# Optimization experiments

Hardware: AMD Instinct MI355X
Metric: run time of the kernel (lower is better)

Reference implementation:

```python
import jax, jax.numpy as jnp
import numpy as np

N, E, ND, D = 100000, 200000, 128, 32


def linear_bn(x, W, g, b, eps=1e-5):
    # Linear (no bias) followed by BatchNorm1d in training mode (batch stats)
    y = x @ W
    mu = jnp.mean(y, axis=0)
    var = jnp.var(y, axis=0)
    return g * (y - mu) * jax.lax.rsqrt(var + eps) + b


def setup_inputs() -> dict:
    key = jax.random.key(0)
    ks = jax.random.split(key, 16)
    s = 0.05
    return {
        "node": jax.random.normal(ks[0], (N, ND), jnp.float32),
        "edge_index": jax.random.randint(ks[1], (E, 2), 0, N, jnp.int64),
        "edge": jax.random.normal(ks[2], (E, D), jnp.float32),
        "hidden": jax.random.normal(ks[3], (1, E, D), jnp.float32),
        "W1": jax.random.normal(ks[4], (2 * ND, 256), jnp.float32) * s,
        "g1": jnp.ones((256,), jnp.float32), "b1": jnp.zeros((256,), jnp.float32),
        "W2": jax.random.normal(ks[5], (256, 256), jnp.float32) * s,
        "g2": jnp.ones((256,), jnp.float32), "b2": jnp.zeros((256,), jnp.float32),
        "W3": jax.random.normal(ks[6], (256, 128), jnp.float32) * s,
        "g3": jnp.ones((128,), jnp.float32), "b3": jnp.zeros((128,), jnp.float32),
        "W4": jax.random.normal(ks[7], (128, D * D), jnp.float32) * s,
        "g4": jnp.ones((D * D,), jnp.float32), "b4": jnp.zeros((D * D,), jnp.float32),
        "bias": jax.random.uniform(ks[8], (D,), jnp.float32, -1.0 / np.sqrt(D), 1.0 / np.sqrt(D)),
        "W_ih": jax.random.normal(ks[9], (3 * D, D), jnp.float32) * s,
        "W_hh": jax.random.normal(ks[10], (3 * D, D), jnp.float32) * s,
        "b_ih": jnp.zeros((3 * D,), jnp.float32),
        "b_hh": jnp.zeros((3 * D,), jnp.float32),
    }


def reference(node, edge_index, edge, hidden, W1, g1, b1, W2, g2, b2, W3, g3, b3,
              W4, g4, b4, bias, W_ih, W_hh, b_ih, b_hh):
    num_edge, edge_dim = edge.shape
    # gather endpoint node features and concat -> [E, 2*node_dim]
    x_ij = jnp.concatenate([node[edge_index[:, 0]], node[edge_index[:, 1]]], axis=1)
    h = jax.nn.relu(linear_bn(x_ij, W1, g1, b1))
    h = jax.nn.relu(linear_bn(h, W2, g2, b2))
    h = jax.nn.relu(linear_bn(h, W3, g3, b3))
    A = linear_bn(h, W4, g4, b4).reshape(num_edge, edge_dim, edge_dim)
    # per-edge small matmul: [E,1,D] @ [E,D,D] -> [E,D]
    message = jnp.einsum('ed,edf->ef', edge, A)
    message = jax.nn.relu(message + bias)
    # single-step GRU (seq_len=1, edges as batch)
    h0 = hidden[0]
    gi = message @ W_ih.T + b_ih
    gh = h0 @ W_hh.T + b_hh
    i_r, i_z, i_n = jnp.split(gi, 3, axis=1)
    h_r, h_z, h_n = jnp.split(gh, 3, axis=1)
    r = jax.nn.sigmoid(i_r + h_r)
    z = jax.nn.sigmoid(i_z + h_z)
    n = jnp.tanh(i_n + r * h_n)
    h_new = (1.0 - z) * n + z * h0
    return h_new, h_new[None]
```

## Files before the change

kernel.cpp:

```cpp
#include <hip/hip_runtime.h>
#include <hip/hip_fp16.h>

#define NE 200000
#define NT 6250
#define NT64 3125
#define GRAM_BLOCKS 512

__device__ float g_st[21248];
__device__ unsigned short g_c4h[1024];
__device__ int g_flag64;

#define SUM1 (&g_st[0])
#define SQ1  (&g_st[256])
#define SUM2 (&g_st[512])
#define SQ2  (&g_st[768])
#define SUM3 (&g_st[1024])
#define SQ3  (&g_st[1152])
#define GMAT (&g_st[1280])
#define CS3  (&g_st[17664])
#define A1   (&g_st[17792])
#define C1   (&g_st[18048])
#define A2   (&g_st[18304])
#define C2   (&g_st[18560])
#define A3   (&g_st[18816])
#define C3   (&g_st[18944])
#define A4   (&g_st[19072])
#define C4   (&g_st[20096])

typedef unsigned short u16;
typedef _Float16 f16x8 __attribute__((ext_vector_type(8)));
typedef float f32x4 __attribute__((ext_vector_type(4)));

__device__ __forceinline__ f32x4 mfma16(f16x8 a, f16x8 b, f32x4 c) {
  return __builtin_amdgcn_mfma_f32_16x16x32_f16(a, b, c, 0, 0, 0);
}
__device__ __forceinline__ u16 f2h(float x) {
  __half h = __float2half_rn(x);
  return *reinterpret_cast<u16*>(&h);
}
__device__ __forceinline__ float h2f(u16 s) {
  __half h = *reinterpret_cast<__half*>(&s);
  return __half2float(h);
}
__device__ __forceinline__ float relu_np(float t) { return (t < 0.f) ? 0.f : t; }
__device__ __forceinline__ unsigned packh2(float a, float b) {
  return (unsigned)f2h(a) | ((unsigned)f2h(b) << 16);
}

__global__ void GraphConv2_16518444221042_kernel(float* __restrict__ out,
                                                 float v, int n) {
  int i = blockIdx.x * 256 + threadIdx.x;
  if (i < n) out[i] = v;
}

__global__ void k_init(const int* __restrict__ e) {
  int i = blockIdx.x * 256 + threadIdx.x;
  if (i < 17792) g_st[i] = 0.f;
  if (i == 0) {
    int allz = 1;
    for (int k = 1; k < 128; k += 2) allz &= (e[k] == 0);
    g_flag64 = allz;
  }
}

__global__ void k_packA(const float* __restrict__ W1,
                        const float* __restrict__ W2,
                        const float* __restrict__ W3,
                        u16* __restrict__ dst) {
  int i = blockIdx.x * 256 + threadIdx.x;
  if (i >= 163840) return;
  float v;
  if (i < 65536) {
    int n = i >> 8, k = i & 255;
    v = W1[k * 256 + n];
  } else if (i < 131072) {
    int i2 = i - 65536, n = i2 >> 8, k = i2 & 255;
    v = W2[k * 256 + n];
  } else {
    int i2 = i - 131072, n = i2 >> 8, k = i2 & 255;
    v = W3[k * 128 + n];
  }
  dst[i] = f2h(v);
}

__global__ void k_packB(const float* __restrict__ W4,
                        const float* __restrict__ Wih,
                        const float* __restrict__ Whh,
                        u16* __restrict__ dst) {
  int i = blockIdx.x * 256 + threadIdx.x;
  if (i >= 137216) return;
  float v;
  if (i < 131072) {
    int n = i >> 7, k = i & 127;
    v = W4[(size_t)k * 1024 + n];
  } else if (i < 134144) {
    v = Wih[i - 131072];
  } else {
    v = Whh[i - 134144];
  }
  dst[i] = f2h(v);
}

__global__ void k_finalize(const float* __restrict__ g,
                           const float* __restrict__ b, int which, int C) {
  int j = threadIdx.x;
  if (j < C) {
    const float* sum = (which == 1) ? SUM1 : (which == 2) ? SUM2 : SUM3;
    const float* sq  = (which == 1) ? SQ1 : (which == 2) ? SQ2 : SQ3;
    float* aa = (which == 1) ? A1 : (which == 2) ? A2 : A3;
    float* cc = (which == 1) ? C1 : (which == 2) ? C2 : C3;
    const float invE = 1.f / (float)NE;
    float mu = sum[j] * invE;
    float var = fmaf(-mu, mu, sq[j] * invE);
    float s = rsqrtf(var + 1e-5f);
    float av = g[j] * s;
    aa[j] = av;
    cc[j] = fmaf(-av, mu, b[j]);
  }
}

__global__ __launch_bounds__(64) void k_finalize4(
    const float* __restrict__ W4, const float* __restrict__ g4,
    const float* __restrict__ b4) {
  __shared__ float wsh[128];
  const int lane = threadIdx.x;
  const float invE = 1.f / (float)NE;
  for (int j = blockIdx.x; j < 1024; j += gridDim.x) {
    float w0 = W4[lane * 1024 + j];
    float w1 = W4[(lane + 64) * 1024 + j];
    wsh[lane] = w0;
    wsh[lane + 64] = w1;
    __syncthreads();
    float s0 = 0.f, s1 = 0.f;
#pragma unroll 8
    for (int k = 0; k < 128; ++k) {
      float wk = wsh[k];
      s0 = fmaf(GMAT[lane * 128 + k], wk, s0);
      s1 = fmaf(GMAT[(lane + 64) * 128 + k], wk, s1);
    }
    float acc = w0 * s0 + w1 * s1;
    float mac = CS3[lane] * w0 + CS3[lane + 64] * w1;
#pragma unroll
    for (int off = 32; off > 0; off >>= 1) {
      acc += __shfl_down(acc, off);
      mac += __shfl_down(mac, off);
    }
    if (lane == 0) {
      float mu = mac * invE;
      float var = fmaf(-mu, mu, acc * invE);
      float s = rsqrtf(var + 1e-5f);
      float av = g4[j] * s;
      A4[j] = av;
      float cv = fmaf(-av, mu, b4[j]);
      C4[j] = cv;
      g_c4h[(j & 31) * 32 + (j >> 5)] = f2h(cv);
    }
    __syncthreads();
  }
}

template <int L>
__global__ __launch_bounds__(512) void k_gemmP(
    const float* __restrict__ node, const int* __restrict__ eidx,
    const u16* __restrict__ Yin, const u16* __restrict__ Wt,
    u16* __restrict__ Yout) {
  constexpr int CN = (L == 3) ? 128 : 256;
  constexpr int CTW = CN / 128;
  constexpr int LDH = 264;
  __shared__ __align__(16) u16 H[64 * LDH];
  __shared__ float csum_s[CN], csq_s[CN];
  __shared__ int idx_s[128];
  const int tid = threadIdx.x;
  float* SUMo = (L == 1) ? SUM1 : (L == 2) ? SUM2 : SUM3;
  float* SQo  = (L == 1) ? SQ1 : (L == 2) ? SQ2 : SQ3;
  const float* Ain = (L == 2) ? A1 : A2;
  const float* Cin = (L == 2) ? C1 : C2;

  const int l = tid & 63, w = tid >> 6;
  const int lr = l & 15, lg = l >> 4;

  f16x8 bfr[CTW][8];
#pragma unroll
  for (int c = 0; c < CTW; ++c)
#pragma unroll
    for (int kb = 0; kb < 8; ++kb)
      bfr[c][kb] = *(const f16x8*)&Wt[(size_t)((w * CTW + c) * 16 + lr) * 256 +
                                      kb * 32 + lg * 8];

  if (tid < CN) { csum_s[tid] = 0.f; csq_s[tid] = 0.f; }
  float sreg[CTW] = {}, qreg[CTW] = {};

  for (int t = blockIdx.x; t < NT64; t += gridDim.x) {
    const int r0 = t * 64;
    __syncthreads();
    if constexpr (L == 1) {
      if (tid < 128) {
        const int is64 = g_flag64;
        int m = tid & 63, sel = tid >> 6;
        int j = (r0 + m) * 2 + sel;
        int v = is64 ? eidx[j * 2] : eidx[j];
        v = v < 0 ? 0 : (v > 99999 ? 99999 : v);
        idx_s[sel * 64 + m] = v;
      }
      __syncthreads();
#pragma unroll
      for (int i = 0; i < 8; ++i) {
        int idx = tid + i * 512;
        int row = idx >> 6, col = (idx & 63) * 4;
        int sel = col >> 7, kc = col & 127;
        float4 v =
            *(const float4*)&node[(size_t)idx_s[sel * 64 + row] * 128 + kc];
        uint2 pk;
        pk.x = packh2(v.x, v.y);
        pk.y = packh2(v.z, v.w);
        *(uint2*)&H[row * LDH + col] = pk;
      }
    } else {
#pragma unroll
      for (int i = 0; i < 4; ++i) {
        int idx = tid + i * 512;
        int row = idx >> 5, col = (idx & 31) * 8;
        uint4 ld = *(const uint4*)&Yin[(size_t)(r0 + row) * 256 + col];
        const u16* sp = (const u16*)&ld;
        uint4 o;
        unsigned po[4];
#pragma unroll
        for (int p = 0; p < 4; ++p) {
          float v0 = relu_np(fmaf(Ain[col + 2 * p], h2f(sp[2 * p]),
                                  Cin[col + 2 * p]));
          float v1 = relu_np(fmaf(Ain[col + 2 * p + 1], h2f(sp[2 * p + 1]),
                                  Cin[col + 2 * p + 1]));
          po[p] = packh2(v0, v1);
        }
        o.x = po[0]; o.y = po[1]; o.z = po[2]; o.w = po[3];
        *(uint4*)&H[row * LDH + col] = o;
      }
    }
    __syncthreads();

    f32x4 acc[4][CTW] = {};
#pragma unroll
    for (int kb = 0; kb < 8; ++kb) {
      f16x8 a[4];
#pragma unroll
      for (int rt = 0; rt < 4; ++rt)
        a[rt] = *(const f16x8*)&H[(rt * 16 + lr) * LDH + kb * 32 + lg * 8];
#pragma unroll
      for (int c = 0; c < CTW; ++c)
#pragma unroll
        for (int rt = 0; rt < 4; ++rt)
          acc[rt][c] = mfma16(a[rt], bfr[c][kb], acc[rt][c]);
    }

#pragma unroll
    for (int c = 0; c < CTW; ++c) {
      const int col = (w * CTW + c) * 16 + lr;
#pragma unroll
      for (int rt = 0; rt < 4; ++rt)
#pragma unroll
        for (int r = 0; r < 4; ++r) {
          float v = acc[rt][c][r];
          sreg[c] += v;
          qreg[c] = fmaf(v, v, qreg[c]);
          int row = rt * 16 + lg * 4 + r;
          Yout[(size_t)(r0 + row) * CN + col] = f2h(v);
        }
    }
  }

  __syncthreads();
#pragma unroll
  for (int c = 0; c < CTW; ++c) {
    const int col = (w * CTW + c) * 16 + lr;
    atomicAdd(&csum_s[col], sreg[c]);
    atomicAdd(&csq_s[col], qreg[c]);
  }
  __syncthreads();
  if (tid < CN) {
    atomicAdd(&SUMo[tid], csum_s[tid]);
    atomicAdd(&SQo[tid], csq_s[tid]);
  }
}

__global__ __launch_bounds__(256, 2) void k_gram_m(const u16* __restrict__ y3g,
                                                   float* __restrict__ pg) {
  __shared__ u16 h3T[128 * 40];
  __shared__ float cred[128];
  const int tid = threadIdx.x;
  const int l = tid & 63, w = tid >> 6;
  const int lr = l & 15, lg = l >> 4;
  const int c4 = (tid & 31) * 4;
  const int rb = tid >> 5;
  f32x4 acc[2][8] = {};
  float csc[4] = {0.f, 0.f, 0.f, 0.f};

  for (int t = blockIdx.x; t < NT; t += gridDim.x) {
    const size_t r0 = (size_t)t * 32;
    __syncthreads();
#pragma unroll
    for (int i = 0; i < 4; ++i) {
      int row = rb + i * 8;
      ushort4 v = *(const ushort4*)&y3g[(r0 + row) * 128 + c4];
      float h[4];
      h[0] = relu_np(fmaf(A3[c4 + 0], h2f(v.x), C3[c4 + 0]));
      h[1] = relu_np(fmaf(A3[c4 + 1], h2f(v.y), C3[c4 + 1]));
      h[2] = relu_np(fmaf(A3[c4 + 2], h2f(v.z), C3[c4 + 2]));
      h[3] = relu_np(fmaf(A3[c4 + 3], h2f(v.w), C3[c4 + 3]));
#pragma unroll
      for (int j = 0; j < 4; ++j) {
        csc[j] += h[j];
        int col = c4 + j;
        int swz = ((col >> 2) & 3) << 3;
        h3T[col * 40 + (row ^ swz)] = f2h(h[j]);
      }
    }
    __syncthreads();
    f16x8 bfr[8];
#pragma unroll
    for (int tj = 0; tj < 8; ++tj) {
      int col = tj * 16 + lr;
      int swz = ((col >> 2) & 3) << 3;
      bfr[tj] = *(const f16x8*)&h3T[col * 40 + ((lg * 8) ^ swz)];
    }
#pragma unroll
    for (int ri = 0; ri < 2; ++ri) {
      f16x8 a = bfr[w * 2 + ri];
#pragma unroll
      for (int tj = 0; tj < 8; ++tj)
        acc[ri][tj] = mfma16(a, bfr[tj], acc[ri][tj]);
    }
  }
  float* my = pg + (size_t)blockIdx.x * 16384;
#pragma unroll
  for (int ri = 0; ri < 2; ++ri)
#pragma unroll
    for (int tj = 0; tj < 8; ++tj)
#pragma unroll
      for (int r = 0; r < 4; ++r) {
        int row = (w * 2 + ri) * 16 + lg * 4 + r, col = tj * 16 + lr;
        my[row * 128 + col] = acc[ri][tj][r];
      }
  if (tid < 128) cred[tid] = 0.f;
  __syncthreads();
#pragma unroll
  for (int j = 0; j < 4; ++j) atomicAdd(&cred[c4 + j], csc[j]);
  __syncthreads();
  if (tid < 128) atomicAdd(&CS3[tid], cred[tid]);
}

__global__ void k_gramred(const float* __restrict__ pg) {
  int g = blockIdx.x * 256 + threadIdx.x;
  float s = 0.f;
  for (int p = 0; p < GRAM_BLOCKS; ++p) s += pg[(size_t)p * 16384 + g];
  GMAT[g] = s;
}

__global__ __launch_bounds__(256, 4) void k_final64(
    const u16* __restrict__ y3g, const u16* __restrict__ w4t,
    const u16* __restrict__ wihh, const u16* __restrict__ whhh,
    const float* __restrict__ edge, const float* __restrict__ hidden,
    const float* __restrict__ bias, const float* __restrict__ bih,
    const float* __restrict__ bhh, float* __restrict__ out) {
  __shared__ __align__(16) u16 H3[64 * 136];
  __shared__ __align__(16) u16 SLAB[32 * 136];
  __shared__ __align__(16) u16 EDS[64 * 40];
  float* OUTBUF = (float*)H3;
  u16* MSGu = H3 + 4096;
  const int tid = threadIdx.x;
  const size_t r0 = (size_t)blockIdx.x * 64;

#pragma unroll
  for (int i = 0; i < 8; ++i) {
    int idx = tid + i * 256;
    int row = idx >> 5, col = (idx & 31) * 4;
    ushort4 v = *(const ushort4*)&y3g[(r0 + row) * 128 + col];
    float h0 = relu_np(fmaf(A3[col + 0], h2f(v.x), C3[col + 0]));
    float h1 = relu_np(fmaf(A3[col + 1], h2f(v.y), C3[col + 1]));
    float h2v = relu_np(fmaf(A3[col + 2], h2f(v.z), C3[col + 2]));
    float h3v = relu_np(fmaf(A3[col + 3], h2f(v.w), C3[col + 3]));
    uint2 pk;
    pk.x = packh2(h0, h1);
    pk.y = packh2(h2v, h3v);
    *(uint2*)&H3[row * 136 + col] = pk;
  }
#pragma unroll
  for (int i = 0; i < 2; ++i) {
    int idx = tid + i * 256;
    int row = idx >> 3, col = (idx & 7) * 4;
    float4 ev = *(const float4*)&edge[(r0 + row) * 32 + col];
    uint2 pe;
    pe.x = packh2(ev.x, ev.y);
    pe.y = packh2(ev.z, ev.w);
    *(uint2*)&EDS[row * 40 + col] = pe;
  }
  __syncthreads();

  const int l = tid & 63, w = tid >> 6;
  const int lr = l & 15, lg = l >> 4;
  f16x8 af[4];
#pragma unroll
  for (int kb = 0; kb < 4; ++kb)
    af[kb] = *(const f16x8*)&H3[(w * 16 + lr) * 136 + kb * 32 + lg * 8];

  float mp[4][2] = {};
  for (int cg = 0; cg < 32; ++cg) {
    __syncthreads();
    {
      int c = tid >> 3, ch = tid & 7;
#pragma unroll
      for (int q = 0; q < 2; ++q) {
        int kk = (ch + q * 8) * 8;
        *(uint4*)&SLAB[c * 136 + kk] =
            *(const uint4*)&w4t[(size_t)(cg * 32 + c) * 128 + kk];
      }
    }
    __syncthreads();
#pragma unroll
    for (int ci = 0; ci < 2; ++ci) {
      f16x8 b[4];
#pragma unroll
      for (int kb = 0; kb < 4; ++kb)
        b[kb] = *(const f16x8*)&SLAB[(ci * 16 + lr) * 136 + kb * 32 + lg * 8];
      const float a4v = A4[cg * 32 + ci * 16 + lr];
      f32x4 acc = {0.f, 0.f, 0.f, 0.f};
#pragma unroll
      for (int kb = 0; kb < 4; ++kb) acc = mfma16(af[kb], b[kb], acc);
#pragma unroll
      for (int r = 0; r < 4; ++r) {
        int e = w * 16 + lg * 4 + r;
        float ed = h2f(EDS[e * 40 + cg]);
        mp[r][ci] = fmaf(ed * a4v, acc[r], mp[r][ci]);
      }
    }
  }

  f32x4 m0[2];
  {
    f16x8 ae = *(const f16x8*)&EDS[(w * 16 + lr) * 40 + lg * 8];
#pragma unroll
    for (int ci = 0; ci < 2; ++ci) {
      f16x8 bc = *(const f16x8*)&g_c4h[(ci * 16 + lr) * 32 + lg * 8];
      f32x4 z = {0.f, 0.f, 0.f, 0.f};
      m0[ci] = mfma16(ae, bc, z);
    }
  }
#pragma unroll
  for (int ci = 0; ci < 2; ++ci)
#pragma unroll
    for (int r = 0; r < 4; ++r) {
      int e = w * 16 + lg * 4 + r;
      int f = ci * 16 + lr;
      float v = relu_np(mp[r][ci] + m0[ci][r] + bias[f]);
      MSGu[e * 40 + f] = f2h(v);
    }
  __syncthreads();

  f16x8 am = *(const f16x8*)&MSGu[(w * 16 + lr) * 40 + lg * 8];
  f16x8 ah;
  {
    int e = w * 16 + lr;
    float4 h0a = *(const float4*)&hidden[(r0 + e) * 32 + lg * 8];
    float4 h0b = *(const float4*)&hidden[(r0 + e) * 32 + lg * 8 + 4];
    union { unsigned u[4]; f16x8 h; } uu;
    uu.u[0] = packh2(h0a.x, h0a.y);
    uu.u[1] = packh2(h0a.z, h0a.w);
    uu.u[2] = packh2(h0b.x, h0b.y);
    uu.u[3] = packh2(h0b.z, h0b.w);
    ah = uu.h;
  }
  f32x4 gi[6], gh[6];
#pragma unroll
  for (int ct = 0; ct < 6; ++ct) {
    f16x8 bi = *(const f16x8*)&wihh[(ct * 16 + lr) * 32 + lg * 8];
    f16x8 bh = *(const f16x8*)&whhh[(ct * 16 + lr) * 32 + lg * 8];
    f32x4 z = {0.f, 0.f, 0.f, 0.f};
    gi[ct] = mfma16(am, bi, z);
    gh[ct] = mfma16(ah, bh, z);
  }
#pragma unroll
  for (int r = 0; r < 4; ++r) {
    int e = w * 16 + lg * 4 + r;
#pragma unroll
    for (int hf = 0; hf < 2; ++hf) {
      int f = hf * 16 + lr;
      float xr = gi[hf][r] + bih[f];
      float xz = gi[2 + hf][r] + bih[32 + f];
      float xn = gi[4 + hf][r] + bih[64 + f];
      float hr = gh[hf][r] + bhh[f];
      float hz = gh[2 + hf][r] + bhh[32 + f];
      float hn = gh[4 + hf][r] + bhh[64 + f];
      float rg = 1.f / (1.f + __expf(-(xr + hr)));
      float zg = 1.f / (1.f + __expf(-(xz + hz)));
      float ng = tanhf(fmaf(rg, hn, xn));
      float h0v = hidden[(r0 + e) * 32 + f];
      OUTBUF[e * 32 + f] = fmaf(zg, h0v - ng, ng);
    }
  }
  __syncthreads();
#pragma unroll
  for (int i = 0; i < 2; ++i) {
    int off = tid * 4 + i * 1024;
    size_t g = r0 * 32 + off;
    float4 v = *(const float4*)&OUTBUF[off];
    *(float4*)&out[g] = v;
    *(float4*)&out[(size_t)NE * 32 + g] = v;
  }
}

extern "C" void kernel_launch(void* const* d_in, const int* in_sizes, int n_in,
                              void* d_out, int out_size, void* d_ws,
                              size_t ws_size, hipStream_t stream) {
  float* out = (float*)d_out;

  static const int EXP[21] = {
      12800000, 400000, 6400000, 6400000,
      65536, 256, 256, 65536, 256, 256, 32768, 128, 128,
      131072, 1024, 1024, 32, 3072, 3072, 96, 96};
  int bad = -1;
  if (n_in != 21) bad = 25;
  else
    for (int i = 0; i < 21; ++i)
      if (in_sizes[i] != EXP[i]) { bad = i; break; }
  if (bad < 0 && out_size != 12800000) bad = 22;
  const size_t Y1B = (size_t)NE * 256 * 2;
  if (bad < 0 && (!d_ws || ws_size < 2 * Y1B)) bad = 24;
  if (bad >= 0) {
    float code = 3.0e7f + (float)bad * 1.0e6f;
    GraphConv2_16518444221042_kernel<<<(out_size + 255) / 256, 256, 0, stream>>>(
        out, code, out_size);
    return;
  }

  const float* node   = (const float*)d_in[0];
  const int*   eidx   = (const int*)d_in[1];
  const float* edge   = (const float*)d_in[2];
  const float* hidden = (const float*)d_in[3];
  const float* W1 = (const float*)d_in[4];
  const float* g1 = (const float*)d_in[5];
  const float* b1 = (const float*)d_in[6];
  const float* W2 = (const float*)d_in[7];
  const float* g2 = (const float*)d_in[8];
  const float* b2 = (const float*)d_in[9];
  const float* W3 = (const float*)d_in[10];
  const float* g3 = (const float*)d_in[11];
  const float* b3 = (const float*)d_in[12];
  const float* W4 = (const float*)d_in[13];
  const float* g4 = (const float*)d_in[14];
  const float* b4 = (const float*)d_in[15];
  const float* bias = (const float*)d_in[16];
  const float* Wih = (const float*)d_in[17];
  const float* Whh = (const float*)d_in[18];
  const float* bih = (const float*)d_in[19];
  const float* bhh = (const float*)d_in[20];

  u16* y1 = (u16*)d_ws;
  u16* y2 = (u16*)d_ws + (size_t)NE * 256;
  u16* y3 = (u16*)d_ws;

  u16* pkA = (u16*)d_out;
  u16* w1t = pkA;
  u16* w2t = pkA + 65536;
  u16* w3t = pkA + 131072;
  u16* w4t  = y2;
  u16* wihh = y2 + 131072;
  u16* whhh = y2 + 134144;
  float* pgram = (float*)(y2 + 2097152);

  k_init<<<70, 256, 0, stream>>>(eidx);
  k_packA<<<640, 256, 0, stream>>>(W1, W2, W3, pkA);

  k_gemmP<1><<<512, 512, 0, stream>>>(node, eidx, nullptr, w1t, y1);
  k_finalize<<<1, 256, 0, stream>>>(g1, b1, 1, 256);
  k_gemmP<2><<<512, 512, 0, stream>>>(nullptr, nullptr, y1, w2t, y2);
  k_finalize<<<1, 256, 0, stream>>>(g2, b2, 2, 256);
  k_gemmP<3><<<512, 512, 0, stream>>>(nullptr, nullptr, y2, w3t, y3);
  k_finalize<<<1, 256, 0, stream>>>(g3, b3, 3, 128);
  k_packB<<<537, 256, 0, stream>>>(W4, Wih, Whh, y2);
  k_gram_m<<<GRAM_BLOCKS, 256, 0, stream>>>(y3, pgram);
  k_gramred<<<64, 256, 0, stream>>>(pgram);
  k_finalize4<<<128, 64, 0, stream>>>(W4, g4, b4);
  k_final64<<<NT64, 256, 0, stream>>>(y3, w4t, wihh, whhh, edge, hidden,
                                      bias, bih, bhh, out);
}
```

Before: 429.4 us.

## Double-buffer GEMM input tiles with register prefetch of the next tile

The layer GEMM kernel now keeps two shared-memory H buffers and prefetches the next tile's global data (node gathers or previous-layer activations) into registers while the current tile is computed. One barrier per iteration is dropped and the idx_s shared staging is removed: each thread reads its edge indices directly, so edge_index is loaded redundantly per element. The aim is to hide global load latency behind the MFMA work, at the cost of more registers and twice the LDS footprint, which may lower occupancy.

Result: no change. 424.1 us (-1.2%).

```diff
diff --git a/kernel.cpp b/kernel.cpp
--- a/kernel.cpp
+++ b/kernel.cpp
@@ -167,9 +167,8 @@
   constexpr int CN = (L == 3) ? 128 : 256;
   constexpr int CTW = CN / 128;
   constexpr int LDH = 264;
-  __shared__ __align__(16) u16 H[64 * LDH];
+  __shared__ __align__(16) u16 H[2][64 * LDH];
   __shared__ float csum_s[CN], csq_s[CN];
-  __shared__ int idx_s[128];
   const int tid = threadIdx.x;
   float* SUMo = (L == 1) ? SUM1 : (L == 2) ? SUM2 : SUM3;
   float* SQo  = (L == 1) ? SQ1 : (L == 2) ? SQ2 : SQ3;
@@ -178,6 +177,7 @@
 
   const int l = tid & 63, w = tid >> 6;
   const int lr = l & 15, lg = l >> 4;
+  const int is64 = g_flag64;
 
   f16x8 bfr[CTW][8];
 #pragma unroll
@@ -190,38 +190,52 @@
   if (tid < CN) { csum_s[tid] = 0.f; csq_s[tid] = 0.f; }
   float sreg[CTW] = {}, qreg[CTW] = {};
 
-  for (int t = blockIdx.x; t < NT64; t += gridDim.x) {
-    const int r0 = t * 64;
-    __syncthreads();
+  float4 ldf[8];
+  uint4 ldi[4];
+
+  {
+    const int r0 = blockIdx.x * 64;
     if constexpr (L == 1) {
-      if (tid < 128) {
-        const int is64 = g_flag64;
-        int m = tid & 63, sel = tid >> 6;
-        int j = (r0 + m) * 2 + sel;
-        int v = is64 ? eidx[j * 2] : eidx[j];
-        v = v < 0 ? 0 : (v > 99999 ? 99999 : v);
-        idx_s[sel * 64 + m] = v;
-      }
-      __syncthreads();
 #pragma unroll
       for (int i = 0; i < 8; ++i) {
         int idx = tid + i * 512;
         int row = idx >> 6, col = (idx & 63) * 4;
         int sel = col >> 7, kc = col & 127;
-        float4 v =
-            *(const float4*)&node[(size_t)idx_s[sel * 64 + row] * 128 + kc];
-        uint2 pk;
-        pk.x = packh2(v.x, v.y);
-        pk.y = packh2(v.z, v.w);
-        *(uint2*)&H[row * LDH + col] = pk;
+        int j = (r0 + row) * 2 + sel;
+        int v = is64 ? eidx[j * 2] : eidx[j];
+        v = v < 0 ? 0 : (v > 99999 ? 99999 : v);
+        ldf[i] = *(const float4*)&node[(size_t)v * 128 + kc];
       }
     } else {
 #pragma unroll
       for (int i = 0; i < 4; ++i) {
         int idx = tid + i * 512;
         int row = idx >> 5, col = (idx & 31) * 8;
-        uint4 ld = *(const uint4*)&Yin[(size_t)(r0 + row) * 256 + col];
-        const u16* sp = (const u16*)&ld;
+        ldi[i] = *(const uint4*)&Yin[(size_t)(r0 + row) * 256 + col];
+      }
+    }
+  }
+
+  int cur = 0;
+  for (int t = blockIdx.x; t < NT64; t += gridDim.x) {
+    const int r0 = t * 64;
+    const int tn = t + gridDim.x;
+    if constexpr (L == 1) {
+#pragma unroll
+      for (int i = 0; i < 8; ++i) {
+        int idx = tid + i * 512;
+        int row = idx >> 6, col = (idx & 63) * 4;
+        uint2 pk;
+        pk.x = packh2(ldf[i].x, ldf[i].y);
+        pk.y = packh2(ldf[i].z, ldf[i].w);
+        *(uint2*)&H[cur][row * LDH + col] = pk;
+      }
+    } else {
+#pragma unroll
+      for (int i = 0; i < 4; ++i) {
+        int idx = tid + i * 512;
+        int row = idx >> 5, col = (idx & 31) * 8;
+        const u16* sp = (const u16*)&ldi[i];
         uint4 o;
         unsigned po[4];
 #pragma unroll
@@ -233,7 +247,29 @@
           po[p] = packh2(v0, v1);
         }
         o.x = po[0]; o.y = po[1]; o.z = po[2]; o.w = po[3];
-        *(uint4*)&H[row * LDH + col] = o;
+        *(uint4*)&H[cur][row * LDH + col] = o;
+      }
+    }
+    if (tn < NT64) {
+      const int rn = tn * 64;
+      if constexpr (L == 1) {
+#pragma unroll
+        for (int i = 0; i < 8; ++i) {
+          int idx = tid + i * 512;
+          int row = idx >> 6, col = (idx & 63) * 4;
+          int sel = col >> 7, kc = col & 127;
+          int j = (rn + row) * 2 + sel;
+          int v = is64 ? eidx[j * 2] : eidx[j];
+          v = v < 0 ? 0 : (v > 99999 ? 99999 : v);
+          ldf[i] = *(const float4*)&node[(size_t)v * 128 + kc];
+        }
+      } else {
+#pragma unroll
+        for (int i = 0; i < 4; ++i) {
+          int idx = tid + i * 512;
+          int row = idx >> 5, col = (idx & 31) * 8;
+          ldi[i] = *(const uint4*)&Yin[(size_t)(rn + row) * 256 + col];
+        }
       }
     }
     __syncthreads();
@@ -244,7 +280,7 @@
       f16x8 a[4];
 #pragma unroll
       for (int rt = 0; rt < 4; ++rt)
-        a[rt] = *(const f16x8*)&H[(rt * 16 + lr) * LDH + kb * 32 + lg * 8];
+        a[rt] = *(const f16x8*)&H[cur][(rt * 16 + lr) * LDH + kb * 32 + lg * 8];
 #pragma unroll
       for (int c = 0; c < CTW; ++c)
 #pragma unroll
@@ -266,6 +302,7 @@
           Yout[(size_t)(r0 + row) * CN + col] = f2h(v);
         }
     }
+    cur ^= 1;
   }
 
   __syncthreads();
```
